# Kernel tuning notes

Hardware: AMD Instinct MI355X
Metric: run time of the kernel (lower is better)

Reference implementation:

```python
import jax, jax.numpy as jnp
import numpy as np

B, S, H, L, NH, FF, V, T = 32, 512, 768, 6, 12, 3072, 30522, 7
DH = H // NH


def setup_inputs():
    key = jax.random.key(0)
    ks = iter(jax.random.split(key, 32))

    def w(shape, scale=0.02):
        return jax.random.normal(next(ks), shape, jnp.float32) * scale

    inp = {
        "word_emb": w((V, H)),
        "pos_emb": w((S, H)),
        "emb_ln_s": jnp.ones((H,), jnp.float32),
        "emb_ln_b": jnp.zeros((H,), jnp.float32),
        "attn_qw": w((L, H, H)), "attn_qb": jnp.zeros((L, H), jnp.float32),
        "attn_kw": w((L, H, H)), "attn_kb": jnp.zeros((L, H), jnp.float32),
        "attn_vw": w((L, H, H)), "attn_vb": jnp.zeros((L, H), jnp.float32),
        "attn_ow": w((L, H, H)), "attn_ob": jnp.zeros((L, H), jnp.float32),
        "ln1_s": jnp.ones((L, H), jnp.float32), "ln1_b": jnp.zeros((L, H), jnp.float32),
        "ffn_w1": w((L, H, FF)), "ffn_b1": jnp.zeros((L, FF), jnp.float32),
        "ffn_w2": w((L, FF, H)), "ffn_b2": jnp.zeros((L, H), jnp.float32),
        "ln2_s": jnp.ones((L, H), jnp.float32), "ln2_b": jnp.zeros((L, H), jnp.float32),
        "cls_w": w((H, T)), "cls_b": jnp.zeros((T,), jnp.float32),
        "crf_start": w((T,), 0.1), "crf_end": w((T,), 0.1), "crf_trans": w((T, T), 0.1),
    }
    lengths = jax.random.randint(next(ks), (B,), S // 2, S + 1)
    attention_mask = (jnp.arange(S)[None, :] < lengths[:, None]).astype(jnp.int32)
    raw_labels = jax.random.randint(next(ks), (B, S), 0, T)
    inp["input_ids"] = jax.random.randint(next(ks), (B, S), 0, V)
    inp["attention_mask"] = attention_mask
    inp["labels"] = jnp.where(attention_mask == 1, raw_labels, -100)  # -100 = ignore
    return inp


def _layer_norm(x, s, b, eps=1e-12):
    m = x.mean(-1, keepdims=True)
    v = ((x - m) ** 2).mean(-1, keepdims=True)
    return (x - m) / jnp.sqrt(v + eps) * s + b


def _forward(params, input_ids, attention_mask, labels):
    (word_emb, pos_emb, emb_ln_s, emb_ln_b, attn_qw, attn_qb, attn_kw, attn_kb,
     attn_vw, attn_vb, attn_ow, attn_ob, ln1_s, ln1_b, ffn_w1, ffn_b1, ffn_w2,
     ffn_b2, ln2_s, ln2_b, cls_w, cls_b, crf_start, crf_end, crf_trans) = params
    amask = attention_mask.astype(bool)            # [B,S]
    # DistilBERT embeddings (word + position, then LayerNorm; dropout = identity in eval)
    x = word_emb[input_ids] + pos_emb[None, :, :]  # [B,S,H]
    x = _layer_norm(x, emb_ln_s, emb_ln_b)
    neg = jnp.finfo(x.dtype).min
    for i in range(L):  # 6 structurally distinct transformer layers
        q = (x @ attn_qw[i] + attn_qb[i]).reshape(B, S, NH, DH).transpose(0, 2, 1, 3)
        k = (x @ attn_kw[i] + attn_kb[i]).reshape(B, S, NH, DH).transpose(0, 2, 1, 3)
        v = (x @ attn_vw[i] + attn_vb[i]).reshape(B, S, NH, DH).transpose(0, 2, 1, 3)
        scores = jnp.einsum('bhqd,bhkd->bhqk', q, k) / jnp.sqrt(jnp.float32(DH))
        scores = jnp.where(amask[:, None, None, :], scores, neg)
        probs = jax.nn.softmax(scores, axis=-1)
        ctx = jnp.einsum('bhqk,bhkd->bhqd', probs, v).transpose(0, 2, 1, 3).reshape(B, S, H)
        x = _layer_norm(x + ctx @ attn_ow[i] + attn_ob[i], ln1_s[i], ln1_b[i])
        h = jax.nn.gelu(x @ ffn_w1[i] + ffn_b1[i], approximate=False)
        x = _layer_norm(x + h @ ffn_w2[i] + ffn_b2[i], ln2_s[i], ln2_b[i])
    emissions = x @ cls_w + cls_b                  # [B,S,T]

    # ---- CRF negative mean log-likelihood (torchcrf semantics, batch_first) ----
    mask = (labels != -100).at[:, 0].set(True)     # [B,S] bool
    safe = jnp.where(mask, labels, 0)
    safe = safe.at[:, 0].set(jnp.clip(safe[:, 0], 0, T - 1))
    b_idx = jnp.arange(B)
    # numerator: score of the given tag sequence
    emit = jnp.take_along_axis(emissions, safe[:, :, None], axis=2)[:, :, 0]  # [B,S]
    trans = crf_trans[safe[:, :-1], safe[:, 1:]]                              # [B,S-1]
    num = crf_start[safe[:, 0]] + emit[:, 0]
    num = num + jnp.sum(jnp.where(mask[:, 1:], trans + emit[:, 1:], 0.0), axis=1)
    seq_ends = mask.sum(axis=1) - 1
    num = num + crf_end[safe[b_idx, seq_ends]]
    # denominator: forward algorithm (logsumexp recursion over timesteps)
    alpha0 = crf_start[None, :] + emissions[:, 0]  # [B,T]

    def step(alpha, xs):
        em_t, m_t = xs                              # [B,T], [B]
        nxt = jax.nn.logsumexp(alpha[:, :, None] + crf_trans[None] + em_t[:, None, :], axis=1)
        return jnp.where(m_t[:, None], nxt, alpha), None

    alpha, _ = jax.lax.scan(step, alpha0,
                            (emissions[:, 1:].transpose(1, 0, 2), mask[:, 1:].T))
    denom = jax.nn.logsumexp(alpha + crf_end[None, :], axis=1)
    return -(num - denom).mean()  # reduction='mean', returned negated


def reference(word_emb, pos_emb, emb_ln_s, emb_ln_b, attn_qw, attn_qb, attn_kw,
              attn_kb, attn_vw, attn_vb, attn_ow, attn_ob, ln1_s, ln1_b, ffn_w1,
              ffn_b1, ffn_w2, ffn_b2, ln2_s, ln2_b, cls_w, cls_b, crf_start,
              crf_end, crf_trans, input_ids, attention_mask, labels):
    params = (word_emb, pos_emb, emb_ln_s, emb_ln_b, attn_qw, attn_qb, attn_kw,
              attn_kb, attn_vw, attn_vb, attn_ow, attn_ob, ln1_s, ln1_b, ffn_w1,
              ffn_b1, ffn_w2, ffn_b2, ln2_s, ln2_b, cls_w, cls_b, crf_start,
              crf_end, crf_trans)
    return _forward(params, input_ids, attention_mask, labels)
```

## Files before the change

### kernel.cpp

```cpp
#include <hip/hip_runtime.h>

constexpr int cB = 32, cS = 512, cH = 768, cL = 6, cNH = 12, cFF = 3072, cT = 7;
constexpr int cM = cB * cS;
constexpr int cDH = cH / cNH;
constexpr int cQS = 2304;

#define DEVI __device__ __forceinline__

typedef __attribute__((ext_vector_type(8))) short bh8_t;
typedef __attribute__((ext_vector_type(4))) float f4_t;

DEVI unsigned short f2bf(float f) {
  unsigned int u = __float_as_uint(f);
  return (unsigned short)((u + 0x7fffu + ((u >> 16) & 1u)) >> 16);
}
DEVI float bf2f(unsigned short h) { return __uint_as_float(((unsigned int)h) << 16); }

typedef __attribute__((address_space(1))) void* gas_t;
typedef __attribute__((address_space(3))) void* las_t;
DEVI void async16(void* lds, const void* g) {
  __builtin_amdgcn_global_load_lds((gas_t)g, (las_t)lds, 16, 0, 0);
}

struct WtransArgs { const float* src[6]; };

__global__ void wtrans_all(WtransArgs args, unsigned short* __restrict__ out) {
  const int m = blockIdx.z;
  const int K = (m == 5) ? cFF : cH;
  const int N = (m == 4) ? cFF : cH;
  int n0, k0;
  if (m < 4) {
    if (blockIdx.x >= 24) return;
    n0 = blockIdx.x * 32; k0 = blockIdx.y * 32;
  } else if (m == 4) {
    n0 = blockIdx.x * 32; k0 = blockIdx.y * 32;
  } else {
    k0 = blockIdx.x * 32; n0 = blockIdx.y * 32;
  }
  const int woffs[6] = {0, 589824, 1179648, 1769472, 2359296, 4718592};
  const float* in = args.src[m];
  unsigned short* o = out + woffs[m];
  __shared__ float tile[32][33];
  const int tx = threadIdx.x, ty = threadIdx.y;
#pragma unroll
  for (int i = 0; i < 4; i++)
    tile[ty + i * 8][tx] = in[(size_t)(k0 + ty + i * 8) * N + n0 + tx];
  __syncthreads();
#pragma unroll
  for (int i = 0; i < 4; i++)
    o[(size_t)(n0 + ty + i * 8) * K + k0 + tx] = f2bf(tile[tx][ty + i * 8]);
}

__global__ void concat_bias(const float* __restrict__ qb, const float* __restrict__ kb,
                            const float* __restrict__ vb, float* __restrict__ out) {
  const int c = blockIdx.x * 256 + threadIdx.x;
  if (c < cQS)
    out[c] = c < cH ? qb[c] : (c < 2 * cH ? kb[c - cH] : vb[c - 2 * cH]);
}

template <bool RESID, bool GELU, bool OUTB>
__global__ __launch_bounds__(256) void gemm_bf16(
    const unsigned short* __restrict__ A, const unsigned short* __restrict__ Bt,
    const float* __restrict__ bias, const float* resid,
    float* outf, unsigned short* __restrict__ outb, int N, int K) {
  __shared__ __align__(16) unsigned short As[128 * 64];
  __shared__ __align__(16) unsigned short Bs[128 * 64];
  const int tid = threadIdx.x;
  const int lane = tid & 63;
  const int wave = tid >> 6;
  const int wm = wave >> 1, wn = wave & 1;
  const int quad = lane >> 4, col = lane & 15;
  const int m0 = blockIdx.y * 128;
  const int n0 = blockIdx.x * 128;

  f4_t acc[4][4] = {};

  const int srow = tid >> 3;
  const int sgld = (tid & 7) ^ (srow & 7);
  const unsigned short* gA = A + (size_t)(m0 + srow) * K + sgld * 8;
  const unsigned short* gB = Bt + (size_t)(n0 + srow) * K + sgld * 8;
  unsigned short* lA = As + tid * 8;
  unsigned short* lB = Bs + tid * 8;

  int offA[2][4], offB[2][4];
#pragma unroll
  for (int ks = 0; ks < 2; ks++) {
#pragma unroll
    for (int t = 0; t < 4; t++) {
      const int rA = wm * 64 + t * 16 + col;
      const int rB = wn * 64 + t * 16 + col;
      offA[ks][t] = rA * 64 + (((ks * 4 + quad) ^ (rA & 7)) << 3);
      offB[ks][t] = rB * 64 + (((ks * 4 + quad) ^ (rB & 7)) << 3);
    }
  }

  for (int k0 = 0; k0 < K; k0 += 64) {
#pragma unroll
    for (int i = 0; i < 4; i++)
      async16(lA + i * 2048, gA + k0 + (size_t)(i * 32) * K);
#pragma unroll
    for (int i = 0; i < 4; i++)
      async16(lB + i * 2048, gB + k0 + (size_t)(i * 32) * K);
    __syncthreads();
#pragma unroll
    for (int ks = 0; ks < 2; ks++) {
      bh8_t af[4], bf[4];
#pragma unroll
      for (int t = 0; t < 4; t++) af[t] = *(const bh8_t*)(As + offA[ks][t]);
#pragma unroll
      for (int t = 0; t < 4; t++) bf[t] = *(const bh8_t*)(Bs + offB[ks][t]);
#pragma unroll
      for (int mi = 0; mi < 4; mi++)
#pragma unroll
        for (int ni = 0; ni < 4; ni++)
          acc[mi][ni] = __builtin_amdgcn_mfma_f32_16x16x32_bf16(af[mi], bf[ni],
                                                                acc[mi][ni], 0, 0, 0);
    }
    __syncthreads();
  }

#pragma unroll
  for (int mi = 0; mi < 4; mi++) {
    const int row = m0 + wm * 64 + mi * 16 + (quad << 2);
#pragma unroll
    for (int ni = 0; ni < 4; ni++) {
      const int coln = n0 + wn * 64 + ni * 16 + col;
      const float bv = bias[coln];
#pragma unroll
      for (int r = 0; r < 4; r++) {
        const size_t idx = (size_t)(row + r) * N + coln;
        float v = acc[mi][ni][r] + bv;
        if (RESID) v += resid[idx];
        if (GELU) v = 0.5f * v * (1.0f + erff(v * 0.70710678118654752f));
        if (OUTB) outb[idx] = f2bf(v);
        else outf[idx] = v;
      }
    }
  }
}

__global__ __launch_bounds__(256) void embed_ln(
    const int* __restrict__ ids, const float* __restrict__ wemb,
    const float* __restrict__ pemb, const float* __restrict__ g,
    const float* __restrict__ be, float* __restrict__ xo,
    unsigned short* __restrict__ xbo) {
  const int token = blockIdx.x;
  const int tid = threadIdx.x;
  const int id = ids[token];
  const int pos = token & (cS - 1);
  const float* wr = wemb + (size_t)id * cH;
  const float* pr = pemb + (size_t)pos * cH;
  float v[3];
#pragma unroll
  for (int i = 0; i < 3; i++) v[i] = wr[tid + i * 256] + pr[tid + i * 256];
  float s = v[0] + v[1] + v[2];
  float s2 = v[0] * v[0] + v[1] * v[1] + v[2] * v[2];
#pragma unroll
  for (int off = 32; off; off >>= 1) { s += __shfl_xor(s, off); s2 += __shfl_xor(s2, off); }
  __shared__ float sa[4], sb[4];
  if ((tid & 63) == 0) { sa[tid >> 6] = s; sb[tid >> 6] = s2; }
  __syncthreads();
  s = sa[0] + sa[1] + sa[2] + sa[3];
  s2 = sb[0] + sb[1] + sb[2] + sb[3];
  const float mean = s * (1.0f / cH);
  const float rstd = rsqrtf(s2 * (1.0f / cH) - mean * mean + 1e-12f);
  float* xr = xo + (size_t)token * cH;
  unsigned short* xbr = xbo + (size_t)token * cH;
#pragma unroll
  for (int i = 0; i < 3; i++) {
    const int c = tid + i * 256;
    const float nv = (v[i] - mean) * rstd * g[c] + be[c];
    xr[c] = nv;
    xbr[c] = f2bf(nv);
  }
}

__global__ __launch_bounds__(256) void ln_fused(
    float* __restrict__ x, const float* __restrict__ g,
    const float* __restrict__ be, unsigned short* __restrict__ xbo) {
  const int token = blockIdx.x;
  const int tid = threadIdx.x;
  float* row = x + (size_t)token * cH;
  float v[3];
#pragma unroll
  for (int i = 0; i < 3; i++) v[i] = row[tid + i * 256];
  float s = v[0] + v[1] + v[2];
  float s2 = v[0] * v[0] + v[1] * v[1] + v[2] * v[2];
#pragma unroll
  for (int off = 32; off; off >>= 1) { s += __shfl_xor(s, off); s2 += __shfl_xor(s2, off); }
  __shared__ float sa[4], sb[4];
  if ((tid & 63) == 0) { sa[tid >> 6] = s; sb[tid >> 6] = s2; }
  __syncthreads();
  s = sa[0] + sa[1] + sa[2] + sa[3];
  s2 = sb[0] + sb[1] + sb[2] + sb[3];
  const float mean = s * (1.0f / cH);
  const float rstd = rsqrtf(s2 * (1.0f / cH) - mean * mean + 1e-12f);
  unsigned short* xbr = xbo + (size_t)token * cH;
#pragma unroll
  for (int i = 0; i < 3; i++) {
    const int c = tid + i * 256;
    const float nv = (v[i] - mean) * rstd * g[c] + be[c];
    row[c] = nv;
    xbr[c] = f2bf(nv);
  }
}

__global__ __launch_bounds__(256, 2) void attn_mfma(
    const unsigned short* __restrict__ qkv, const int* __restrict__ amask,
    unsigned short* __restrict__ ctxb) {
  __shared__ __align__(16) unsigned short Ks[128 * 64];
  __shared__ __align__(16) unsigned short Vt[64 * 128];
  __shared__ __align__(16) unsigned short Ps[4 * 32 * 136];
  __shared__ int lensh[4];

  const int tid = threadIdx.x, lane = tid & 63, wave = tid >> 6;
  const int quad = lane >> 4, col = lane & 15;
  const int wg = blockIdx.x;
  const int qb = wg & 3, h = (wg >> 2) % cNH, b = wg / (4 * cNH);
  const int q0 = qb * 128 + wave * 32;

  const unsigned short* qg = qkv;
  const unsigned short* kg = qkv + cH;
  const unsigned short* vg = qkv + 2 * cH;

  const int* mrow = amask + b * cS;
  int c = mrow[tid] + mrow[tid + 256];
#pragma unroll
  for (int off = 32; off; off >>= 1) c += __shfl_xor(c, off);
  if (lane == 0) lensh[wave] = c;
  __syncthreads();
  const int len = lensh[0] + lensh[1] + lensh[2] + lensh[3];

  const unsigned short* qbase = qg + (size_t)(b * cS + q0) * cQS + h * cDH;
  bh8_t qf[2][2];
#pragma unroll
  for (int mi = 0; mi < 2; mi++)
#pragma unroll
    for (int ks = 0; ks < 2; ks++)
      qf[mi][ks] = *(const bh8_t*)(qbase + (size_t)(mi * 16 + col) * cQS + ks * 32 + quad * 8);

  float mr[2][4], lr[2][4];
  f4_t o[2][4] = {};
#pragma unroll
  for (int mi = 0; mi < 2; mi++)
#pragma unroll
    for (int r = 0; r < 4; r++) { mr[mi][r] = -3.0e38f; lr[mi][r] = 0.0f; }

  unsigned short* Pw = Ps + wave * (32 * 136);

  for (int k0 = 0; k0 < cS; k0 += 128) {
    if (k0 >= len) break;
    __syncthreads();
    const unsigned short* kb = kg + (size_t)(b * cS + k0) * cQS + h * cDH;
    const unsigned short* vb = vg + (size_t)(b * cS + k0) * cQS + h * cDH;
#pragma unroll
    for (int i = 0; i < 4; i++) {
      const int chunk = i * 256 + tid;
      const int key = chunk >> 3;
      const int ld = (chunk & 7) ^ (key & 7);
      async16(Ks + (size_t)(i * 256 + wave * 64) * 8, kb + (size_t)key * cQS + ld * 8);
    }
#pragma unroll
    for (int i = 0; i < 4; i++) {
      const int chunk = i * 256 + tid;
      const int key = chunk >> 3;
      const int ld = chunk & 7;
      const int bk = key >> 3;
      bh8_t vv = *(const bh8_t*)(vb + (size_t)key * cQS + ld * 8);
      unsigned short vs[8];
      *(bh8_t*)vs = vv;
#pragma unroll
      for (int j = 0; j < 8; j++) {
        const int d = ld * 8 + j;
        const int pb = bk ^ j ^ ld;
        Vt[d * 128 + pb * 8 + (key & 7)] = vs[j];
      }
    }
    __syncthreads();

    f4_t s[2][8];
#pragma unroll
    for (int mi = 0; mi < 2; mi++)
#pragma unroll
      for (int n = 0; n < 8; n++) s[mi][n] = f4_t{0.f, 0.f, 0.f, 0.f};
#pragma unroll
    for (int n = 0; n < 8; n++) {
      const int r = n * 16 + col;
#pragma unroll
      for (int ks = 0; ks < 2; ks++) {
        const int phys = (ks * 4 + quad) ^ (col & 7);
        bh8_t kf = *(const bh8_t*)(Ks + (size_t)r * 64 + phys * 8);
        s[0][n] = __builtin_amdgcn_mfma_f32_16x16x32_bf16(qf[0][ks], kf, s[0][n], 0, 0, 0);
        s[1][n] = __builtin_amdgcn_mfma_f32_16x16x32_bf16(qf[1][ks], kf, s[1][n], 0, 0, 0);
      }
    }
#pragma unroll
    for (int n = 0; n < 8; n++) {
      const bool valid = (k0 + n * 16 + col) < len;
#pragma unroll
      for (int mi = 0; mi < 2; mi++)
#pragma unroll
        for (int r = 0; r < 4; r++)
          s[mi][n][r] = valid ? s[mi][n][r] * 0.125f : -3.0e38f;
    }
#pragma unroll
    for (int mi = 0; mi < 2; mi++)
#pragma unroll
      for (int r = 0; r < 4; r++) {
        float v = s[mi][0][r];
#pragma unroll
        for (int n = 1; n < 8; n++) v = fmaxf(v, s[mi][n][r]);
#pragma unroll
        for (int off = 1; off < 16; off <<= 1) v = fmaxf(v, __shfl_xor(v, off));
        const float nm = fmaxf(mr[mi][r], v);
        const float alpha = __expf(mr[mi][r] - nm);
        float rs = 0.0f;
#pragma unroll
        for (int n = 0; n < 8; n++) {
          const float p = __expf(s[mi][n][r] - nm);
          s[mi][n][r] = p;
          rs += p;
        }
#pragma unroll
        for (int off = 1; off < 16; off <<= 1) rs += __shfl_xor(rs, off);
        lr[mi][r] = lr[mi][r] * alpha + rs;
        mr[mi][r] = nm;
#pragma unroll
        for (int nd = 0; nd < 4; nd++) o[mi][nd][r] *= alpha;
      }
#pragma unroll
    for (int mi = 0; mi < 2; mi++)
#pragma unroll
      for (int n = 0; n < 8; n++)
#pragma unroll
        for (int r = 0; r < 4; r++)
          Pw[(mi * 16 + quad * 4 + r) * 136 + n * 16 + col] = f2bf(s[mi][n][r]);
    __syncthreads();
#pragma unroll
    for (int ks = 0; ks < 4; ks++) {
      bh8_t pf[2];
#pragma unroll
      for (int mi = 0; mi < 2; mi++)
        pf[mi] = *(const bh8_t*)(Pw + (size_t)(mi * 16 + col) * 136 + ks * 32 + quad * 8);
#pragma unroll
      for (int nd = 0; nd < 4; nd++) {
        const int d = nd * 16 + col;
        const int pb = (ks * 4 + quad) ^ (d & 7) ^ (d >> 3);
        bh8_t vf = *(const bh8_t*)(Vt + (size_t)d * 128 + pb * 8);
        o[0][nd] = __builtin_amdgcn_mfma_f32_16x16x32_bf16(pf[0], vf, o[0][nd], 0, 0, 0);
        o[1][nd] = __builtin_amdgcn_mfma_f32_16x16x32_bf16(pf[1], vf, o[1][nd], 0, 0, 0);
      }
    }
  }

#pragma unroll
  for (int mi = 0; mi < 2; mi++)
#pragma unroll
    for (int r = 0; r < 4; r++) {
      const float inv = 1.0f / lr[mi][r];
      const int q = q0 + mi * 16 + quad * 4 + r;
      unsigned short* orow = ctxb + (size_t)(b * cS + q) * cH + h * cDH;
#pragma unroll
      for (int nd = 0; nd < 4; nd++) orow[nd * 16 + col] = f2bf(o[mi][nd][r] * inv);
    }
}

__global__ __launch_bounds__(256) void cls_head(
    const float* __restrict__ x, const float* __restrict__ w,
    const float* __restrict__ cb, float* __restrict__ em) {
  const int token = blockIdx.x * 4 + (threadIdx.x >> 6);
  const int lane = threadIdx.x & 63;
  const float* xr = x + (size_t)token * cH;
  float p[cT] = {};
  for (int k = lane; k < cH; k += 64) {
    const float xv = xr[k];
    const float* wr = w + k * cT;
#pragma unroll
    for (int t = 0; t < cT; t++) p[t] += xv * wr[t];
  }
#pragma unroll
  for (int t = 0; t < cT; t++) {
    float r = p[t];
#pragma unroll
    for (int off = 32; off; off >>= 1) r += __shfl_xor(r, off);
    if (lane == t) em[(size_t)token * cT + t] = r + cb[t];
  }
}

__global__ __launch_bounds__(1024) void crf(
    const float* __restrict__ em, const int* __restrict__ labels,
    const float* __restrict__ cstart, const float* __restrict__ cend,
    const float* __restrict__ ctrans, float* __restrict__ out) {
  const int b = blockIdx.x;
  const int tid = threadIdx.x;
  const int wave = tid >> 6, lane = tid & 63;
  const int* lab = labels + b * cS;
  const float* eb = em + (size_t)b * cS * cT;

  __shared__ float mats[16][49];
  __shared__ float mbuf[8][49];
  __shared__ int slen;
  __shared__ float snum;
  if (tid == 0) { slen = 0; snum = 0.0f; }
  __syncthreads();

  if (tid < cS) {
    const int valid = (tid == 0) || (lab[tid] != -100);
    const unsigned long long bal = __ballot(valid);
    if (lane == 0) atomicAdd(&slen, __popcll(bal));
  }
  __syncthreads();
  const int len = slen;

  {
    float np = 0.0f;
    if (tid >= 1 && tid < len)
      np = ctrans[lab[tid - 1] * cT + lab[tid]] + eb[tid * cT + lab[tid]];
#pragma unroll
    for (int off = 32; off; off >>= 1) np += __shfl_xor(np, off);
    if (lane == 0) atomicAdd(&snum, np);
  }

  const int ii = (lane < 49) ? lane / 7 : 0;
  const int jj = (lane < 49) ? lane % 7 : 0;
  const int i7 = ii * 7;
  float trk[cT];
#pragma unroll
  for (int k = 0; k < cT; k++) trk[k] = ctrans[k * cT + jj];

  float Nij = (ii == jj) ? 0.0f : -1.0e30f;
  const int s_beg = 1 + 32 * wave;
  const int s_end = min(s_beg + 32, len);
  for (int s = s_beg; s < s_end; s++) {
    const float ej = eb[s * cT + jj];
    float v[cT];
#pragma unroll
    for (int k = 0; k < cT; k++) v[k] = __shfl(Nij, i7 + k) + trk[k];
    float mx = v[0];
#pragma unroll
    for (int k = 1; k < cT; k++) mx = fmaxf(mx, v[k]);
    float ss = 0.0f;
#pragma unroll
    for (int k = 0; k < cT; k++) ss += __expf(v[k] - mx);
    Nij = mx + __logf(ss) + ej;
  }
  if (lane < 49) mats[wave][lane] = Nij;
  __syncthreads();

  auto compose = [&](const float* Am, const float* Bm) -> float {
    float v[cT];
#pragma unroll
    for (int k = 0; k < cT; k++) v[k] = Am[i7 + k] + Bm[k * 7 + jj];
    float mx = v[0];
#pragma unroll
    for (int k = 1; k < cT; k++) mx = fmaxf(mx, v[k]);
    float ss = 0.0f;
#pragma unroll
    for (int k = 0; k < cT; k++) ss += __expf(v[k] - mx);
    return mx + __logf(ss);
  };
  if (wave < 8 && lane < 49) mbuf[wave][lane] = compose(mats[2 * wave], mats[2 * wave + 1]);
  __syncthreads();
  if (wave < 4 && lane < 49) mats[wave][lane] = compose(mbuf[2 * wave], mbuf[2 * wave + 1]);
  __syncthreads();
  if (wave < 2 && lane < 49) mbuf[wave][lane] = compose(mats[2 * wave], mats[2 * wave + 1]);
  __syncthreads();

  if (wave == 0) {
    float Mij = compose(mbuf[0], mbuf[1]);
    const float a0 = cstart[ii] + eb[ii];
    const float t = a0 + Mij;
    float av[cT];
#pragma unroll
    for (int k = 0; k < cT; k++) av[k] = __shfl(t, k * 7 + lane);
    float mx = av[0];
#pragma unroll
    for (int k = 1; k < cT; k++) mx = fmaxf(mx, av[k]);
    float ss = 0.0f;
#pragma unroll
    for (int k = 0; k < cT; k++) ss += __expf(av[k] - mx);
    const float afin = mx + __logf(ss) + ((lane < cT) ? cend[lane] : 0.0f);
    float dv[cT];
#pragma unroll
    for (int k = 0; k < cT; k++) dv[k] = __shfl(afin, k);
    float dmx = dv[0];
#pragma unroll
    for (int k = 1; k < cT; k++) dmx = fmaxf(dmx, dv[k]);
    float dss = 0.0f;
#pragma unroll
    for (int k = 0; k < cT; k++) dss += __expf(dv[k] - dmx);
    const float denom = dmx + __logf(dss);
    if (lane == 0) {
      const int l0 = lab[0];
      const float num = snum + cstart[l0] + eb[l0] + cend[lab[len - 1]];
      atomicAdd(out, (denom - num) * (1.0f / cB));
    }
  }
}

extern "C" void kernel_launch(void* const* d_in, const int* in_sizes, int n_in,
                              void* d_out, int out_size, void* d_ws, size_t ws_size,
                              hipStream_t stream) {
  const float* word_emb = (const float*)d_in[0];
  const float* pos_emb = (const float*)d_in[1];
  const float* emb_ln_s = (const float*)d_in[2];
  const float* emb_ln_b = (const float*)d_in[3];
  const float* attn_qw = (const float*)d_in[4];
  const float* attn_qb = (const float*)d_in[5];
  const float* attn_kw = (const float*)d_in[6];
  const float* attn_kb = (const float*)d_in[7];
  const float* attn_vw = (const float*)d_in[8];
  const float* attn_vb = (const float*)d_in[9];
  const float* attn_ow = (const float*)d_in[10];
  const float* attn_ob = (const float*)d_in[11];
  const float* ln1_s = (const float*)d_in[12];
  const float* ln1_b = (const float*)d_in[13];
  const float* ffn_w1 = (const float*)d_in[14];
  const float* ffn_b1 = (const float*)d_in[15];
  const float* ffn_w2 = (const float*)d_in[16];
  const float* ffn_b2 = (const float*)d_in[17];
  const float* ln2_s = (const float*)d_in[18];
  const float* ln2_b = (const float*)d_in[19];
  const float* cls_w = (const float*)d_in[20];
  const float* cls_b = (const float*)d_in[21];
  const float* crf_start = (const float*)d_in[22];
  const float* crf_end = (const float*)d_in[23];
  const float* crf_trans = (const float*)d_in[24];
  const int* input_ids = (const int*)d_in[25];
  const int* amask = (const int*)d_in[26];
  const int* labels = (const int*)d_in[27];

  char* ws = (char*)d_ws;
  size_t off = 0;
  auto alloc = [&](size_t bytes) -> void* {
    void* p = ws + off;
    off += (bytes + 255) & ~(size_t)255;
    return p;
  };
  constexpr size_t LW = 7077888;
  unsigned short* Wt = (unsigned short*)alloc(LW * 2);
  float* qkvb = (float*)alloc(cQS * 4);
  float* x = (float*)alloc((size_t)cM * cH * 4);
  unsigned short* xb = (unsigned short*)alloc((size_t)cM * cH * 2);
  unsigned short* un = (unsigned short*)alloc((size_t)cM * cFF * 2);
  unsigned short* qkv = un;
  unsigned short* ctx = un + (size_t)cM * cQS;
  unsigned short* hb = un;
  float* emis = (float*)alloc((size_t)cM * cT * 4);

  hipMemsetAsync(d_out, 0, sizeof(float) * out_size, stream);

  embed_ln<<<cM, 256, 0, stream>>>(input_ids, word_emb, pos_emb, emb_ln_s, emb_ln_b, x, xb);

  for (int i = 0; i < cL; i++) {
    WtransArgs wa;
    wa.src[0] = attn_qw + (size_t)i * cH * cH;
    wa.src[1] = attn_kw + (size_t)i * cH * cH;
    wa.src[2] = attn_vw + (size_t)i * cH * cH;
    wa.src[3] = attn_ow + (size_t)i * cH * cH;
    wa.src[4] = ffn_w1 + (size_t)i * cH * cFF;
    wa.src[5] = ffn_w2 + (size_t)i * cFF * cH;
    wtrans_all<<<dim3(96, 24, 6), dim3(32, 8), 0, stream>>>(wa, Wt);
    concat_bias<<<9, 256, 0, stream>>>(attn_qb + i * cH, attn_kb + i * cH,
                                       attn_vb + i * cH, qkvb);

    gemm_bf16<false, false, true><<<dim3(cQS / 128, cM / 128), 256, 0, stream>>>(
        xb, Wt, qkvb, nullptr, nullptr, qkv, cQS, cH);
    attn_mfma<<<cB * cNH * 4, 256, 0, stream>>>(qkv, amask, ctx);
    gemm_bf16<true, false, false><<<dim3(cH / 128, cM / 128), 256, 0, stream>>>(
        ctx, Wt + 1769472, attn_ob + i * cH, x, x, nullptr, cH, cH);
    ln_fused<<<cM, 256, 0, stream>>>(x, ln1_s + i * cH, ln1_b + i * cH, xb);
    gemm_bf16<false, true, true><<<dim3(cFF / 128, cM / 128), 256, 0, stream>>>(
        xb, Wt + 2359296, ffn_b1 + i * cFF, nullptr, nullptr, hb, cFF, cH);
    gemm_bf16<true, false, false><<<dim3(cH / 128, cM / 128), 256, 0, stream>>>(
        hb, Wt + 4718592, ffn_b2 + i * cH, x, x, nullptr, cH, cFF);
    ln_fused<<<cM, 256, 0, stream>>>(x, ln2_s + i * cH, ln2_b + i * cH, xb);
  }

  cls_head<<<cM / 4, 256, 0, stream>>>(x, cls_w, cls_b, emis);
  crf<<<cB, 1024, 0, stream>>>(emis, labels, crf_start, crf_end, crf_trans, (float*)d_out);
}
```

Baseline: 3.811 ms.

## Shrink GEMM K-tile, swap MFMA operands for vectorized epilogue, approximate GELU erf

The bf16 GEMM now stages 32-wide K tiles instead of 64, with a new XOR swizzle and half the LDS, which allows more resident blocks per CU. The MFMA operands are swapped so each lane holds four consecutive output columns. That lets bias, residual and outputs be read and written with vector loads and stores. GELU's erff is replaced by the Abramowitz-Stegun polynomial approximation with __expf, which is cheaper but slightly less accurate. The cost is twice as many barrier-synchronized loop iterations, each doing less MFMA work.

Result: faster. 3.665 ms (-3.8%).

```diff
diff --git a/kernel.cpp b/kernel.cpp
--- a/kernel.cpp
+++ b/kernel.cpp
@@ -9,12 +9,21 @@
 
 typedef __attribute__((ext_vector_type(8))) short bh8_t;
 typedef __attribute__((ext_vector_type(4))) float f4_t;
+typedef __attribute__((ext_vector_type(4))) unsigned short us4_t;
 
 DEVI unsigned short f2bf(float f) {
   unsigned int u = __float_as_uint(f);
   return (unsigned short)((u + 0x7fffu + ((u >> 16) & 1u)) >> 16);
 }
 DEVI float bf2f(unsigned short h) { return __uint_as_float(((unsigned int)h) << 16); }
+
+DEVI float fast_erff(float x) {
+  const float a = fabsf(x);
+  const float t = 1.0f / (1.0f + 0.3275911f * a);
+  const float y = 1.0f - (((((1.061405429f * t - 1.453152027f) * t) + 1.421413741f) * t
+                            - 0.284496736f) * t + 0.254829592f) * t * __expf(-a * a);
+  return copysignf(y, x);
+}
 
 typedef __attribute__((address_space(1))) void* gas_t;
 typedef __attribute__((address_space(3))) void* las_t;
@@ -63,8 +72,8 @@
     const unsigned short* __restrict__ A, const unsigned short* __restrict__ Bt,
     const float* __restrict__ bias, const float* resid,
     float* outf, unsigned short* __restrict__ outb, int N, int K) {
-  __shared__ __align__(16) unsigned short As[128 * 64];
-  __shared__ __align__(16) unsigned short Bs[128 * 64];
+  __shared__ __align__(16) unsigned short As[128 * 32];
+  __shared__ __align__(16) unsigned short Bs[128 * 32];
   const int tid = threadIdx.x;
   const int lane = tid & 63;
   const int wave = tid >> 6;
@@ -75,65 +84,64 @@
 
   f4_t acc[4][4] = {};
 
-  const int srow = tid >> 3;
-  const int sgld = (tid & 7) ^ (srow & 7);
-  const unsigned short* gA = A + (size_t)(m0 + srow) * K + sgld * 8;
-  const unsigned short* gB = Bt + (size_t)(n0 + srow) * K + sgld * 8;
-  unsigned short* lA = As + tid * 8;
-  unsigned short* lB = Bs + tid * 8;
-
-  int offA[2][4], offB[2][4];
-#pragma unroll
-  for (int ks = 0; ks < 2; ks++) {
-#pragma unroll
-    for (int t = 0; t < 4; t++) {
-      const int rA = wm * 64 + t * 16 + col;
-      const int rB = wn * 64 + t * 16 + col;
-      offA[ks][t] = rA * 64 + (((ks * 4 + quad) ^ (rA & 7)) << 3);
-      offB[ks][t] = rB * 64 + (((ks * 4 + quad) ^ (rB & 7)) << 3);
-    }
-  }
-
-  for (int k0 = 0; k0 < K; k0 += 64) {
-#pragma unroll
-    for (int i = 0; i < 4; i++)
-      async16(lA + i * 2048, gA + k0 + (size_t)(i * 32) * K);
-#pragma unroll
-    for (int i = 0; i < 4; i++)
-      async16(lB + i * 2048, gB + k0 + (size_t)(i * 32) * K);
+  const int rA = tid >> 2;
+  const int cXor = ((tid & 3) ^ ((tid >> 3) & 3)) << 3;
+  const unsigned short* gA = A + (size_t)(m0 + rA) * K + cXor;
+  const unsigned short* gB = Bt + (size_t)(n0 + rA) * K + cXor;
+  unsigned short* lA0 = As + wave * 512;
+  unsigned short* lA1 = As + 2048 + wave * 512;
+  unsigned short* lB0 = Bs + wave * 512;
+  unsigned short* lB1 = Bs + 2048 + wave * 512;
+
+  const int physq = quad ^ ((col >> 1) & 3);
+  const unsigned short* fA[4];
+  const unsigned short* fB[4];
+#pragma unroll
+  for (int t = 0; t < 4; t++) {
+    fA[t] = As + (size_t)(wm * 64 + t * 16 + col) * 32 + physq * 8;
+    fB[t] = Bs + (size_t)(wn * 64 + t * 16 + col) * 32 + physq * 8;
+  }
+
+  for (int k0 = 0; k0 < K; k0 += 32) {
+    async16(lA0, gA + k0);
+    async16(lA1, gA + (size_t)64 * K + k0);
+    async16(lB0, gB + k0);
+    async16(lB1, gB + (size_t)64 * K + k0);
     __syncthreads();
-#pragma unroll
-    for (int ks = 0; ks < 2; ks++) {
-      bh8_t af[4], bf[4];
-#pragma unroll
-      for (int t = 0; t < 4; t++) af[t] = *(const bh8_t*)(As + offA[ks][t]);
-#pragma unroll
-      for (int t = 0; t < 4; t++) bf[t] = *(const bh8_t*)(Bs + offB[ks][t]);
-#pragma unroll
-      for (int mi = 0; mi < 4; mi++)
-#pragma unroll
-        for (int ni = 0; ni < 4; ni++)
-          acc[mi][ni] = __builtin_amdgcn_mfma_f32_16x16x32_bf16(af[mi], bf[ni],
-                                                                acc[mi][ni], 0, 0, 0);
-    }
+    bh8_t af[4], bf[4];
+#pragma unroll
+    for (int t = 0; t < 4; t++) af[t] = *(const bh8_t*)fA[t];
+#pragma unroll
+    for (int t = 0; t < 4; t++) bf[t] = *(const bh8_t*)fB[t];
+#pragma unroll
+    for (int mi = 0; mi < 4; mi++)
+#pragma unroll
+      for (int ni = 0; ni < 4; ni++)
+        acc[mi][ni] = __builtin_amdgcn_mfma_f32_16x16x32_bf16(bf[ni], af[mi],
+                                                              acc[mi][ni], 0, 0, 0);
     __syncthreads();
   }
 
 #pragma unroll
   for (int mi = 0; mi < 4; mi++) {
-    const int row = m0 + wm * 64 + mi * 16 + (quad << 2);
+    const size_t rowbase = (size_t)(m0 + wm * 64 + mi * 16 + col) * N;
 #pragma unroll
     for (int ni = 0; ni < 4; ni++) {
-      const int coln = n0 + wn * 64 + ni * 16 + col;
-      const float bv = bias[coln];
-#pragma unroll
-      for (int r = 0; r < 4; r++) {
-        const size_t idx = (size_t)(row + r) * N + coln;
-        float v = acc[mi][ni][r] + bv;
-        if (RESID) v += resid[idx];
-        if (GELU) v = 0.5f * v * (1.0f + erff(v * 0.70710678118654752f));
-        if (OUTB) outb[idx] = f2bf(v);
-        else outf[idx] = v;
+      const int cb = n0 + wn * 64 + ni * 16 + quad * 4;
+      f4_t v = acc[mi][ni] + *(const f4_t*)(bias + cb);
+      if (RESID) v += *(const f4_t*)(resid + rowbase + cb);
+      if (GELU) {
+#pragma unroll
+        for (int r = 0; r < 4; r++)
+          v[r] = 0.5f * v[r] * (1.0f + fast_erff(v[r] * 0.70710678118654752f));
+      }
+      if (OUTB) {
+        us4_t u;
+#pragma unroll
+        for (int r = 0; r < 4; r++) u[r] = f2bf(v[r]);
+        *(us4_t*)(outb + rowbase + cb) = u;
+      } else {
+        *(f4_t*)(outf + rowbase + cb) = v;
       }
     }
   }
```
